# Kernel tuning notes

Hardware: AMD Instinct MI355X
Metric: run time of the kernel (lower is better)

Reference implementation:

```python
import jax, jax.numpy as jnp
import numpy as np
from jax import lax

D_MODEL = 1024
D_STATE = 16
D_CONV = 4
EXPAND = 2
D_INNER = EXPAND * D_MODEL  # 2048
DT_RANK = -(-D_MODEL // 16)  # ceil = 64
BATCH = 2
T = 1024


def setup_inputs() -> dict:
    key = jax.random.key(0)
    ks = jax.random.split(key, 9)
    s = 0.02
    x = jax.random.normal(ks[0], (BATCH, T, D_MODEL), dtype=jnp.float32)
    W_in = jax.random.normal(ks[1], (D_MODEL, 2 * D_INNER), dtype=jnp.float32) * s
    conv_w = jax.random.normal(ks[2], (D_INNER, D_CONV), dtype=jnp.float32) * 0.2
    conv_b = jax.random.normal(ks[3], (D_INNER,), dtype=jnp.float32) * 0.02
    W_xproj = jax.random.normal(ks[4], (D_INNER, DT_RANK + 2 * D_STATE), dtype=jnp.float32) * s
    W_dt = jax.random.normal(ks[5], (DT_RANK, D_INNER), dtype=jnp.float32) * s
    b_dt = jax.random.normal(ks[6], (D_INNER,), dtype=jnp.float32) * 0.02
    A_log = jnp.broadcast_to(jnp.log(jnp.arange(1, D_STATE + 1, dtype=jnp.float32)), (D_INNER, D_STATE)).copy()
    D_param = jnp.ones((D_INNER,), dtype=jnp.float32)
    W_out = jax.random.normal(ks[7], (D_INNER, D_MODEL), dtype=jnp.float32) * s
    return {"x": x, "W_in": W_in, "conv_w": conv_w, "conv_b": conv_b,
            "W_xproj": W_xproj, "W_dt": W_dt, "b_dt": b_dt,
            "A_log": A_log, "D_param": D_param, "W_out": W_out}


def _silu(u):
    return u * jax.nn.sigmoid(u)


def _forward(x, W_in, conv_w, conv_b, W_xproj, W_dt, b_dt, A_log, D_param, W_out):
    B, Tlen, _ = x.shape
    # in_proj and split into x-branch and gate z
    xz = x @ W_in                                   # (B,T,2*d_inner)
    x_b, z = jnp.split(xz, 2, axis=-1)              # each (B,T,d_inner)
    # causal depthwise conv1d: y[t] = sum_k w[:,k] * x[t-d_conv+1+k]
    xpad = jnp.pad(x_b, ((0, 0), (D_CONV - 1, 0), (0, 0)))
    xc = conv_b
    for k in range(D_CONV):
        xc = xc + xpad[:, k:k + Tlen, :] * conv_w[:, k]
    xc = _silu(xc)                                  # (B,T,d_inner)
    # SSM parameter projections
    proj = xc @ W_xproj                             # (B,T,dt_rank+2*d_state)
    delta_raw = proj[..., :DT_RANK]
    B_in = proj[..., DT_RANK:DT_RANK + D_STATE]     # (B,T,d_state)
    C_in = proj[..., DT_RANK + D_STATE:]            # (B,T,d_state)
    delta = jax.nn.softplus(delta_raw @ W_dt + b_dt)  # (B,T,d_inner)
    A = -jnp.exp(A_log)                             # (d_inner,d_state)
    A_bar = jnp.exp(delta[..., None] * A)           # (B,T,d_inner,d_state)
    Bx = delta[..., None] * B_in[:, :, None, :] * xc[..., None]  # (B,T,d_inner,d_state)

    def step(h, ins):
        a_t, bx_t, c_t, xc_t = ins
        h = a_t * h + bx_t                          # (B,d_inner,d_state)
        y_t = jnp.einsum('bds,bs->bd', h, c_t) + D_param * xc_t
        return h, y_t

    h0 = jnp.zeros((B, D_INNER, D_STATE), dtype=x.dtype)
    ins = (jnp.swapaxes(A_bar, 0, 1), jnp.swapaxes(Bx, 0, 1),
           jnp.swapaxes(C_in, 0, 1), jnp.swapaxes(xc, 0, 1))
    _, ys = lax.scan(step, h0, ins)                 # ys: (T,B,d_inner)
    y = jnp.swapaxes(ys, 0, 1) * _silu(z)           # gated
    return y @ W_out                                # (B,T,d_model)


def reference(x, W_in, conv_w, conv_b, W_xproj, W_dt, b_dt, A_log, D_param, W_out):
    return _forward(x, W_in, conv_w, conv_b, W_xproj, W_dt, b_dt, A_log, D_param, W_out)
```

## Files before the change

### kernel.cpp

```cpp
#include <hip/hip_runtime.h>
#include <math.h>

#define BATCH   2
#define TLEN    1024
#define DMODEL  1024
#define DINNER  2048
#define DSTATE  16
#define DTRANK  64
#define NPROJ   (DTRANK + 2*DSTATE)
#define CH      16
#define NCH     (TLEN / CH)

typedef __attribute__((ext_vector_type(8))) short short8;
typedef __attribute__((ext_vector_type(4))) float f32x4;

__device__ __forceinline__ float siluf(float u) {
    return u / (1.0f + __expf(-u));
}
__device__ __forceinline__ float softplusf(float x) {
    return (x > 20.0f) ? x : log1pf(__expf(x));
}
__device__ __forceinline__ unsigned short f2bf(float f) {
    union { float f; unsigned u; } v; v.f = f;
    unsigned r = v.u + 0x7FFF + ((v.u >> 16) & 1);
    return (unsigned short)(r >> 16);
}

#define GLOAD_LDS16(g, l) \
  __builtin_amdgcn_global_load_lds( \
     (const __attribute__((address_space(1))) unsigned int*)(g), \
     (__attribute__((address_space(3))) unsigned int*)(l), 16, 0, 0)

template<int NFRAG>
__global__ __launch_bounds__(256)
void gemm_bf16(const unsigned short* __restrict__ A,
               const unsigned short* __restrict__ BT,
               float* __restrict__ C, int ldc, int K)
{
    constexpr int BN = NFRAG * 32;
    __shared__ unsigned short As[128 * 32];
    __shared__ unsigned short Bs[BN * 32];

    const int tid  = threadIdx.x;
    const int wid  = tid >> 6;
    const int lane = tid & 63;
    const int brow = blockIdx.y * 128;
    const int bcol = blockIdx.x * BN;
    const int wr = (wid >> 1) * 64;
    const int wc = (wid & 1) * (NFRAG * 16);
    const int lrow = lane & 15;
    const int lk   = (lane >> 4) * 8;

    f32x4 acc[4][NFRAG] = {};

    for (int k0 = 0; k0 < K; k0 += 32) {
        #pragma unroll
        for (int it = 0; it < 2; ++it) {
            const int c = it * 256 + tid;
            const unsigned short* g = A + (size_t)(brow + (c >> 2)) * K + k0 + (c & 3) * 8;
            GLOAD_LDS16(g, As + (size_t)(it * 256 + wid * 64) * 8);
        }
        #pragma unroll
        for (int it = 0; it < BN / 64; ++it) {
            const int c = it * 256 + tid;
            const unsigned short* g = BT + (size_t)(bcol + (c >> 2)) * K + k0 + (c & 3) * 8;
            GLOAD_LDS16(g, Bs + (size_t)(it * 256 + wid * 64) * 8);
        }
        __syncthreads();

        short8 af[4], bfr[NFRAG];
        #pragma unroll
        for (int m = 0; m < 4; ++m)
            af[m] = *(const short8*)(As + (size_t)(wr + m * 16 + lrow) * 32 + lk);
        #pragma unroll
        for (int n = 0; n < NFRAG; ++n)
            bfr[n] = *(const short8*)(Bs + (size_t)(wc + n * 16 + lrow) * 32 + lk);

        #pragma unroll
        for (int m = 0; m < 4; ++m)
            #pragma unroll
            for (int n = 0; n < NFRAG; ++n)
                acc[m][n] = __builtin_amdgcn_mfma_f32_16x16x32_bf16(af[m], bfr[n], acc[m][n], 0, 0, 0);
        __syncthreads();
    }

    const int crow = (lane >> 4) * 4;
    #pragma unroll
    for (int m = 0; m < 4; ++m)
        #pragma unroll
        for (int n = 0; n < NFRAG; ++n) {
            float* cp = C + (size_t)(brow + wr + m * 16 + crow) * ldc + bcol + wc + n * 16 + lrow;
            #pragma unroll
            for (int r = 0; r < 4; ++r)
                cp[(size_t)r * ldc] = acc[m][n][r];
        }
}

template<int EPI>
__global__ __launch_bounds__(256)
void gemm_f32(const float* __restrict__ A, int lda,
              const float* __restrict__ B, int ldb,
              float* __restrict__ C, int ldc,
              int N, int kchunk,
              const float* __restrict__ bias, size_t zstride)
{
    __shared__ float As[16][64 + 4];
    __shared__ float Bs[16][64 + 4];
    const int tid  = threadIdx.x;
    const int brow = blockIdx.y * 64;
    const int bcol = blockIdx.x * 64;
    const int kbeg = blockIdx.z * kchunk;
    C += (size_t)blockIdx.z * zstride;
    const int tr = ((tid >> 4) & 15) << 2;
    const int tc = (tid & 15) << 2;
    const int ar = tid >> 2;
    const int ac = (tid & 3) << 2;
    const int br = tid >> 4;
    const int bc = (tid & 15) << 2;

    float acc[4][4] = {{0.f,0.f,0.f,0.f},{0.f,0.f,0.f,0.f},
                       {0.f,0.f,0.f,0.f},{0.f,0.f,0.f,0.f}};

    for (int k0 = kbeg; k0 < kbeg + kchunk; k0 += 16) {
        float4 av = *(const float4*)(A + (size_t)(brow + ar) * lda + k0 + ac);
        As[ac+0][ar] = av.x; As[ac+1][ar] = av.y;
        As[ac+2][ar] = av.z; As[ac+3][ar] = av.w;

        float4 bv = make_float4(0.f, 0.f, 0.f, 0.f);
        if (bcol + bc < N)
            bv = *(const float4*)(B + (size_t)(k0 + br) * ldb + bcol + bc);
        *(float4*)&Bs[br][bc] = bv;

        __syncthreads();
        #pragma unroll
        for (int k = 0; k < 16; ++k) {
            float4 a4 = *(const float4*)&As[k][tr];
            float4 b4 = *(const float4*)&Bs[k][tc];
            float am[4] = {a4.x, a4.y, a4.z, a4.w};
            float bn[4] = {b4.x, b4.y, b4.z, b4.w};
            #pragma unroll
            for (int m = 0; m < 4; ++m)
                #pragma unroll
                for (int n = 0; n < 4; ++n)
                    acc[m][n] = fmaf(am[m], bn[n], acc[m][n]);
        }
        __syncthreads();
    }

    #pragma unroll
    for (int m = 0; m < 4; ++m) {
        const int gr = brow + tr + m;
        #pragma unroll
        for (int n = 0; n < 4; ++n) {
            const int gc = bcol + tc + n;
            if (gc < N) {
                float v = acc[m][n];
                if (EPI == 1) v = softplusf(v + bias[gc]);
                C[(size_t)gr * ldc + gc] = v;
            }
        }
    }
}

__global__ __launch_bounds__(256)
void reduce8(const float* __restrict__ in, float* __restrict__ out, int n, size_t zstride)
{
    const int i = blockIdx.x * 256 + threadIdx.x;
    if (i >= n) return;
    float s = 0.f;
    #pragma unroll
    for (int z = 0; z < 8; ++z) s += in[(size_t)z * zstride + i];
    out[i] = s;
}

__global__ __launch_bounds__(256)
void cast_rn(const float* __restrict__ in, unsigned short* __restrict__ out)
{
    const int i = blockIdx.x * 256 + threadIdx.x;
    float4 v = ((const float4*)in)[i];
    union { unsigned short u[4]; uint2 v2; } o;
    o.u[0] = f2bf(v.x); o.u[1] = f2bf(v.y); o.u[2] = f2bf(v.z); o.u[3] = f2bf(v.w);
    ((uint2*)out)[i] = o.v2;
}

__global__ __launch_bounds__(256)
void transpose_cast(const float* __restrict__ in, unsigned short* __restrict__ out,
                    int R, int C)
{
    __shared__ float tile[32][33];
    const int tx = threadIdx.x & 31, ty = threadIdx.x >> 5;
    const int c0 = blockIdx.x * 32, r0 = blockIdx.y * 32;
    #pragma unroll
    for (int j = 0; j < 32; j += 8)
        tile[ty + j][tx] = in[(size_t)(r0 + ty + j) * C + c0 + tx];
    __syncthreads();
    #pragma unroll
    for (int j = 0; j < 32; j += 8)
        out[(size_t)(c0 + ty + j) * R + r0 + tx] = f2bf(tile[tx][ty + j]);
}

__global__ __launch_bounds__(256)
void conv_silu(const float* __restrict__ xz, const float* __restrict__ conv_w,
               const float* __restrict__ conv_b, float* __restrict__ xc)
{
    const int idx = blockIdx.x * 256 + threadIdx.x;
    const int d = idx & (DINNER - 1);
    const int t = (idx >> 11) & (TLEN - 1);
    const int b = idx >> 21;

    const float* xb = xz + (size_t)b * TLEN * (2*DINNER) + d;
    float s = conv_b[d];
    const float4 w = *(const float4*)(conv_w + d * 4);
    const float wk[4] = {w.x, w.y, w.z, w.w};
    #pragma unroll
    for (int k = 0; k < 4; ++k) {
        const int tt = t + k - 3;
        if (tt >= 0) s = fmaf(xb[(size_t)tt * (2*DINNER)], wk[k], s);
    }
    xc[idx] = siluf(s);
}

__global__ __launch_bounds__(256)
void scan1(const float* __restrict__ delta, const float* __restrict__ xc,
           const float* __restrict__ proj, const float* __restrict__ A_log,
           float* __restrict__ hloc, float* __restrict__ sumdel)
{
    const int idx = blockIdx.x * 256 + threadIdx.x;
    const int d = idx & (DINNER - 1);
    const int c = (idx >> 11) & (NCH - 1);
    const int b = idx >> 17;

    float Aa[DSTATE];
    #pragma unroll
    for (int s = 0; s < DSTATE; ++s) Aa[s] = -__expf(A_log[d * DSTATE + s]);

    float h[DSTATE];
    #pragma unroll
    for (int s = 0; s < DSTATE; ++s) h[s] = 0.f;
    float sd = 0.f;

    const int t0 = c * CH;
    const float* dptr = delta + ((size_t)(b * TLEN + t0)) * DINNER + d;
    const float* xptr = xc    + ((size_t)(b * TLEN + t0)) * DINNER + d;
    const float* pptr = proj  + ((size_t)(b * TLEN + t0)) * NPROJ;

    for (int t = 0; t < CH; ++t) {
        const float dl = dptr[(size_t)t * DINNER];
        const float xv = xptr[(size_t)t * DINNER];
        const float dx = dl * xv;
        sd += dl;
        #pragma unroll
        for (int s = 0; s < DSTATE; ++s) {
            const float ab = __expf(dl * Aa[s]);
            const float Bv = pptr[t * NPROJ + DTRANK + s];
            h[s] = fmaf(ab, h[s], dx * Bv);
        }
    }
    const size_t base = (((size_t)(b * DINNER + d)) * NCH + c) * DSTATE;
    float4* hp = (float4*)(hloc + base);
    hp[0] = make_float4(h[0],  h[1],  h[2],  h[3]);
    hp[1] = make_float4(h[4],  h[5],  h[6],  h[7]);
    hp[2] = make_float4(h[8],  h[9],  h[10], h[11]);
    hp[3] = make_float4(h[12], h[13], h[14], h[15]);
    sumdel[(size_t)(b * DINNER + d) * NCH + c] = sd;
}

__global__ __launch_bounds__(256)
void scan_combine(const float* __restrict__ hloc, const float* __restrict__ sumdel,
                  const float* __restrict__ A_log, float* __restrict__ hstart)
{
    __shared__ float hl[64 * 17];
    __shared__ float hs[64 * 17];
    const int bd   = blockIdx.x;
    const int d    = bd & (DINNER - 1);
    const int tid  = threadIdx.x;
    const int lane = tid & 63;
    const int w    = tid >> 6;

    const size_t gbase = (size_t)bd * NCH * DSTATE;
    {
        const float4 v = ((const float4*)(hloc + gbase))[tid];
        const int c = tid >> 2, s0 = (tid & 3) * 4;
        hl[c*17 + s0+0] = v.x; hl[c*17 + s0+1] = v.y;
        hl[c*17 + s0+2] = v.z; hl[c*17 + s0+3] = v.w;
    }
    const float sd = sumdel[(size_t)bd * NCH + lane];
    __syncthreads();

    #pragma unroll
    for (int q = 0; q < 4; ++q) {
        const int s = w * 4 + q;
        const float Aa = -__expf(A_log[d * DSTATE + s]);
        float A  = __expf(Aa * sd);
        float Bv = hl[lane*17 + s];
        #pragma unroll
        for (int off = 1; off < 64; off <<= 1) {
            float Ap = __shfl_up(A, off);
            float Bp = __shfl_up(Bv, off);
            if (lane >= off) { Bv = fmaf(A, Bp, Bv); A *= Ap; }
        }
        float hsv = __shfl_up(Bv, 1);
        if (lane == 0) hsv = 0.f;
        hs[lane*17 + s] = hsv;
    }
    __syncthreads();
    {
        const int c = tid >> 2, s0 = (tid & 3) * 4;
        float4 v = make_float4(hs[c*17 + s0+0], hs[c*17 + s0+1],
                               hs[c*17 + s0+2], hs[c*17 + s0+3]);
        ((float4*)(hstart + gbase))[tid] = v;
    }
}

__global__ __launch_bounds__(256)
void scan2(const float* __restrict__ delta, const float* __restrict__ xc,
           const float* __restrict__ proj, const float* __restrict__ A_log,
           const float* __restrict__ D_param, const float* __restrict__ xz,
           const float* __restrict__ hstart, unsigned short* __restrict__ y)
{
    const int idx = blockIdx.x * 256 + threadIdx.x;
    const int d = idx & (DINNER - 1);
    const int c = (idx >> 11) & (NCH - 1);
    const int b = idx >> 17;

    float Aa[DSTATE];
    #pragma unroll
    for (int s = 0; s < DSTATE; ++s) Aa[s] = -__expf(A_log[d * DSTATE + s]);

    float h[DSTATE];
    const size_t hbase = (((size_t)(b * DINNER + d)) * NCH + c) * DSTATE;
    {
        const float4* hp = (const float4*)(hstart + hbase);
        float4 v0 = hp[0], v1 = hp[1], v2 = hp[2], v3 = hp[3];
        h[0]=v0.x; h[1]=v0.y; h[2]=v0.z; h[3]=v0.w;
        h[4]=v1.x; h[5]=v1.y; h[6]=v1.z; h[7]=v1.w;
        h[8]=v2.x; h[9]=v2.y; h[10]=v2.z; h[11]=v2.w;
        h[12]=v3.x; h[13]=v3.y; h[14]=v3.z; h[15]=v3.w;
    }

    const float Dp = D_param[d];
    const int t0 = c * CH;
    const float* dptr = delta + ((size_t)(b * TLEN + t0)) * DINNER + d;
    const float* xptr = xc    + ((size_t)(b * TLEN + t0)) * DINNER + d;
    const float* pptr = proj  + ((size_t)(b * TLEN + t0)) * NPROJ;
    const float* zptr = xz + ((size_t)(b * TLEN + t0)) * (2*DINNER) + DINNER + d;
    unsigned short* yptr = y + ((size_t)(b * TLEN + t0)) * DINNER + d;

    for (int t = 0; t < CH; ++t) {
        const float dl = dptr[(size_t)t * DINNER];
        const float xv = xptr[(size_t)t * DINNER];
        const float dx = dl * xv;
        float yt = 0.f;
        #pragma unroll
        for (int s = 0; s < DSTATE; ++s) {
            const float ab = __expf(dl * Aa[s]);
            const float Bv = pptr[t * NPROJ + DTRANK + s];
            h[s] = fmaf(ab, h[s], dx * Bv);
            const float Cv = pptr[t * NPROJ + DTRANK + DSTATE + s];
            yt = fmaf(h[s], Cv, yt);
        }
        yt = fmaf(Dp, xv, yt);
        const float z = zptr[(size_t)t * (2*DINNER)];
        yptr[(size_t)t * DINNER] = f2bf(yt * siluf(z));
    }
}

extern "C" void kernel_launch(void* const* d_in, const int* in_sizes, int n_in,
                              void* d_out, int out_size, void* d_ws, size_t ws_size,
                              hipStream_t stream)
{
    const float* x      = (const float*)d_in[0];
    const float* W_in   = (const float*)d_in[1];
    const float* conv_w = (const float*)d_in[2];
    const float* conv_b = (const float*)d_in[3];
    const float* W_xproj= (const float*)d_in[4];
    const float* W_dt   = (const float*)d_in[5];
    const float* b_dt   = (const float*)d_in[6];
    const float* A_log  = (const float*)d_in[7];
    const float* D_param= (const float*)d_in[8];
    const float* W_out  = (const float*)d_in[9];
    float* out = (float*)d_out;

    float* ws = (float*)d_ws;
    float* xz     = ws;
    float* xc     = xz     + 8388608;
    float* proj   = xc     + 4194304;
    float* delta  = proj   + 196608;
    float* hloc   = delta  + 4194304;
    float* sumdel = hloc   + 4194304;
    float* hstart = sumdel + 262144;
    float* projp  = hloc;
    unsigned short* x_bf  = (unsigned short*)hstart;
    unsigned short* wt_in = (unsigned short*)(hstart + 1048576);
    unsigned short* yb_bf = (unsigned short*)hloc;
    unsigned short* wt_out= (unsigned short*)(hloc + 2097152);

    dim3 blk(256);

    cast_rn<<<(BATCH*TLEN*DMODEL/4)/256, blk, 0, stream>>>(x, x_bf);
    transpose_cast<<<dim3(2*DINNER/32, DMODEL/32), blk, 0, stream>>>(W_in, wt_in, DMODEL, 2*DINNER);
    gemm_bf16<4><<<dim3(2*DINNER/128, 2048/128), blk, 0, stream>>>(x_bf, wt_in, xz, 2*DINNER, DMODEL);

    conv_silu<<<(BATCH*TLEN*DINNER)/256, blk, 0, stream>>>(xz, conv_w, conv_b, xc);

    gemm_f32<0><<<dim3(2, 2048/64, 8), blk, 0, stream>>>(
        xc, DINNER, W_xproj, NPROJ, projp, NPROJ, NPROJ, DINNER/8, nullptr, 196608);
    reduce8<<<(196608 + 255)/256, blk, 0, stream>>>(projp, proj, 196608, 196608);

    gemm_f32<1><<<dim3(2048/64, 2048/64), blk, 0, stream>>>(
        proj, NPROJ, W_dt, DINNER, delta, DINNER, DINNER, DTRANK, b_dt, 0);

    scan1<<<(BATCH*NCH*DINNER)/256, blk, 0, stream>>>(delta, xc, proj, A_log, hloc, sumdel);
    scan_combine<<<BATCH*DINNER, blk, 0, stream>>>(hloc, sumdel, A_log, hstart);
    transpose_cast<<<dim3(DMODEL/32, DINNER/32), blk, 0, stream>>>(W_out, wt_out, DINNER, DMODEL);
    scan2<<<(BATCH*NCH*DINNER)/256, blk, 0, stream>>>(delta, xc, proj, A_log, D_param, xz, hstart, yb_bf);

    gemm_bf16<2><<<dim3(DMODEL/64, 2048/128), blk, 0, stream>>>(yb_bf, wt_out, out, DMODEL, DINNER);
}
```

Measured before the change: 289.7 us.

## Store xz, xc and delta intermediates in bf16 and remap GEMM blocks per XCD

The large intermediates (in_proj output xz, conv output xc, delta) are now stored as bf16 instead of fp32. This halves the memory traffic of the conv, scan and projection kernels, which are bandwidth-bound. The bf16 GEMM also remaps workgroup IDs so consecutive tiles land on the same XCD for better L2 locality. The cost is lower precision in the scan inputs, which could affect accuracy tolerance.

```diff
diff --git a/kernel.cpp b/kernel.cpp
--- a/kernel.cpp
+++ b/kernel.cpp
@@ -25,27 +25,39 @@
     unsigned r = v.u + 0x7FFF + ((v.u >> 16) & 1);
     return (unsigned short)(r >> 16);
 }
+__device__ __forceinline__ float bf2f(unsigned short u) {
+    union { unsigned u; float f; } v; v.u = (unsigned)u << 16;
+    return v.f;
+}
 
 #define GLOAD_LDS16(g, l) \
   __builtin_amdgcn_global_load_lds( \
      (const __attribute__((address_space(1))) unsigned int*)(g), \
      (__attribute__((address_space(3))) unsigned int*)(l), 16, 0, 0)
 
-template<int NFRAG>
+template<int NFRAG, int OUTBF>
 __global__ __launch_bounds__(256)
 void gemm_bf16(const unsigned short* __restrict__ A,
                const unsigned short* __restrict__ BT,
-               float* __restrict__ C, int ldc, int K)
+               void* __restrict__ Cv, int ldc, int K)
 {
     constexpr int BN = NFRAG * 32;
     __shared__ unsigned short As[128 * 32];
     __shared__ unsigned short Bs[BN * 32];
 
+    const int nwg = gridDim.x * gridDim.y;
+    int id = blockIdx.y * gridDim.x + blockIdx.x;
+    {
+        const int q = nwg >> 3, r = nwg & 7, xcd = id & 7, lid = id >> 3;
+        id = (xcd < r ? xcd * (q + 1) : r * (q + 1) + (xcd - r) * q) + lid;
+    }
+    const int bx = id % gridDim.x, by = id / gridDim.x;
+
     const int tid  = threadIdx.x;
     const int wid  = tid >> 6;
     const int lane = tid & 63;
-    const int brow = blockIdx.y * 128;
-    const int bcol = blockIdx.x * BN;
+    const int brow = by * 128;
+    const int bcol = bx * BN;
     const int wr = (wid >> 1) * 64;
     const int wc = (wid & 1) * (NFRAG * 16);
     const int lrow = lane & 15;
@@ -89,18 +101,22 @@
     for (int m = 0; m < 4; ++m)
         #pragma unroll
         for (int n = 0; n < NFRAG; ++n) {
-            float* cp = C + (size_t)(brow + wr + m * 16 + crow) * ldc + bcol + wc + n * 16 + lrow;
+            const size_t coff = (size_t)(brow + wr + m * 16 + crow) * ldc + bcol + wc + n * 16 + lrow;
             #pragma unroll
-            for (int r = 0; r < 4; ++r)
-                cp[(size_t)r * ldc] = acc[m][n][r];
-        }
-}
-
-template<int EPI>
-__global__ __launch_bounds__(256)
-void gemm_f32(const float* __restrict__ A, int lda,
+            for (int r = 0; r < 4; ++r) {
+                if (OUTBF)
+                    ((unsigned short*)Cv)[coff + (size_t)r * ldc] = f2bf(acc[m][n][r]);
+                else
+                    ((float*)Cv)[coff + (size_t)r * ldc] = acc[m][n][r];
+            }
+        }
+}
+
+template<int EPI, int ABF, int OUTBF>
+__global__ __launch_bounds__(256)
+void gemm_f32(const void* __restrict__ Av, int lda,
               const float* __restrict__ B, int ldb,
-              float* __restrict__ C, int ldc,
+              void* __restrict__ Cv, int ldc,
               int N, int kchunk,
               const float* __restrict__ bias, size_t zstride)
 {
@@ -110,7 +126,7 @@
     const int brow = blockIdx.y * 64;
     const int bcol = blockIdx.x * 64;
     const int kbeg = blockIdx.z * kchunk;
-    C += (size_t)blockIdx.z * zstride;
+    const size_t cofs = (size_t)blockIdx.z * zstride;
     const int tr = ((tid >> 4) & 15) << 2;
     const int tc = (tid & 15) << 2;
     const int ar = tid >> 2;
@@ -122,7 +138,14 @@
                        {0.f,0.f,0.f,0.f},{0.f,0.f,0.f,0.f}};
 
     for (int k0 = kbeg; k0 < kbeg + kchunk; k0 += 16) {
-        float4 av = *(const float4*)(A + (size_t)(brow + ar) * lda + k0 + ac);
+        float4 av;
+        if (ABF) {
+            const unsigned short* Ab = (const unsigned short*)Av;
+            ushort4 t = *(const ushort4*)(Ab + (size_t)(brow + ar) * lda + k0 + ac);
+            av = make_float4(bf2f(t.x), bf2f(t.y), bf2f(t.z), bf2f(t.w));
+        } else {
+            av = *(const float4*)((const float*)Av + (size_t)(brow + ar) * lda + k0 + ac);
+        }
         As[ac+0][ar] = av.x; As[ac+1][ar] = av.y;
         As[ac+2][ar] = av.z; As[ac+3][ar] = av.w;
 
@@ -156,7 +179,10 @@
             if (gc < N) {
                 float v = acc[m][n];
                 if (EPI == 1) v = softplusf(v + bias[gc]);
-                C[(size_t)gr * ldc + gc] = v;
+                if (OUTBF)
+                    ((unsigned short*)Cv)[cofs + (size_t)gr * ldc + gc] = f2bf(v);
+                else
+                    ((float*)Cv)[cofs + (size_t)gr * ldc + gc] = v;
             }
         }
     }
@@ -200,28 +226,28 @@
 }
 
 __global__ __launch_bounds__(256)
-void conv_silu(const float* __restrict__ xz, const float* __restrict__ conv_w,
-               const float* __restrict__ conv_b, float* __restrict__ xc)
+void conv_silu(const unsigned short* __restrict__ xz, const float* __restrict__ conv_w,
+               const float* __restrict__ conv_b, unsigned short* __restrict__ xc)
 {
     const int idx = blockIdx.x * 256 + threadIdx.x;
     const int d = idx & (DINNER - 1);
     const int t = (idx >> 11) & (TLEN - 1);
     const int b = idx >> 21;
 
-    const float* xb = xz + (size_t)b * TLEN * (2*DINNER) + d;
+    const unsigned short* xb = xz + (size_t)b * TLEN * (2*DINNER) + d;
     float s = conv_b[d];
     const float4 w = *(const float4*)(conv_w + d * 4);
     const float wk[4] = {w.x, w.y, w.z, w.w};
     #pragma unroll
     for (int k = 0; k < 4; ++k) {
         const int tt = t + k - 3;
-        if (tt >= 0) s = fmaf(xb[(size_t)tt * (2*DINNER)], wk[k], s);
-    }
-    xc[idx] = siluf(s);
-}
-
-__global__ __launch_bounds__(256)
-void scan1(const float* __restrict__ delta, const float* __restrict__ xc,
+        if (tt >= 0) s = fmaf(bf2f(xb[(size_t)tt * (2*DINNER)]), wk[k], s);
+    }
+    xc[idx] = f2bf(siluf(s));
+}
+
+__global__ __launch_bounds__(256)
+void scan1(const unsigned short* __restrict__ delta, const unsigned short* __restrict__ xc,
            const float* __restrict__ proj, const float* __restrict__ A_log,
            float* __restrict__ hloc, float* __restrict__ sumdel)
 {
@@ -240,13 +266,13 @@
     float sd = 0.f;
 
     const int t0 = c * CH;
-    const float* dptr = delta + ((size_t)(b * TLEN + t0)) * DINNER + d;
-    const float* xptr = xc    + ((size_t)(b * TLEN + t0)) * DINNER + d;
+    const unsigned short* dptr = delta + ((size_t)(b * TLEN + t0)) * DINNER + d;
+    const unsigned short* xptr = xc    + ((size_t)(b * TLEN + t0)) * DINNER + d;
     const float* pptr = proj  + ((size_t)(b * TLEN + t0)) * NPROJ;
 
     for (int t = 0; t < CH; ++t) {
-        const float dl = dptr[(size_t)t * DINNER];
-        const float xv = xptr[(size_t)t * DINNER];
+        const float dl = bf2f(dptr[(size_t)t * DINNER]);
+        const float xv = bf2f(xptr[(size_t)t * DINNER]);
         const float dx = dl * xv;
         sd += dl;
         #pragma unroll
@@ -313,9 +339,9 @@
 }
 
 __global__ __launch_bounds__(256)
-void scan2(const float* __restrict__ delta, const float* __restrict__ xc,
+void scan2(const unsigned short* __restrict__ delta, const unsigned short* __restrict__ xc,
            const float* __restrict__ proj, const float* __restrict__ A_log,
-           const float* __restrict__ D_param, const float* __restrict__ xz,
+           const float* __restrict__ D_param, const unsigned short* __restrict__ xz,
            const float* __restrict__ hstart, unsigned short* __restrict__ y)
 {
     const int idx = blockIdx.x * 256 + threadIdx.x;
@@ -340,15 +366,15 @@
 
     const float Dp = D_param[d];
     const int t0 = c * CH;
-    const float* dptr = delta + ((size_t)(b * TLEN + t0)) * DINNER + d;
-    const float* xptr = xc    + ((size_t)(b * TLEN + t0)) * DINNER + d;
+    const unsigned short* dptr = delta + ((size_t)(b * TLEN + t0)) * DINNER + d;
+    const unsigned short* xptr = xc    + ((size_t)(b * TLEN + t0)) * DINNER + d;
     const float* pptr = proj  + ((size_t)(b * TLEN + t0)) * NPROJ;
-    const float* zptr = xz + ((size_t)(b * TLEN + t0)) * (2*DINNER) + DINNER + d;
+    const unsigned short* zptr = xz + ((size_t)(b * TLEN + t0)) * (2*DINNER) + DINNER + d;
     unsigned short* yptr = y + ((size_t)(b * TLEN + t0)) * DINNER + d;
 
     for (int t = 0; t < CH; ++t) {
-        const float dl = dptr[(size_t)t * DINNER];
-        const float xv = xptr[(size_t)t * DINNER];
+        const float dl = bf2f(dptr[(size_t)t * DINNER]);
+        const float xv = bf2f(xptr[(size_t)t * DINNER]);
         const float dx = dl * xv;
         float yt = 0.f;
         #pragma unroll
@@ -360,7 +386,7 @@
             yt = fmaf(h[s], Cv, yt);
         }
         yt = fmaf(Dp, xv, yt);
-        const float z = zptr[(size_t)t * (2*DINNER)];
+        const float z = bf2f(zptr[(size_t)t * (2*DINNER)]);
         yptr[(size_t)t * DINNER] = f2bf(yt * siluf(z));
     }
 }
@@ -382,38 +408,38 @@
     float* out = (float*)d_out;
 
     float* ws = (float*)d_ws;
-    float* xz     = ws;
-    float* xc     = xz     + 8388608;
-    float* proj   = xc     + 4194304;
-    float* delta  = proj   + 196608;
-    float* hloc   = delta  + 4194304;
-    float* sumdel = hloc   + 4194304;
-    float* hstart = sumdel + 262144;
-    float* projp  = hloc;
-    unsigned short* x_bf  = (unsigned short*)hstart;
-    unsigned short* wt_in = (unsigned short*)(hstart + 1048576);
-    unsigned short* yb_bf = (unsigned short*)hloc;
-    unsigned short* wt_out= (unsigned short*)(hloc + 2097152);
+    unsigned short* xz_bf    = (unsigned short*)ws;
+    unsigned short* xc_bf    = (unsigned short*)(ws + 4194304);
+    float*          proj     = ws + 6291456;
+    unsigned short* delta_bf = (unsigned short*)(ws + 6488064);
+    float*          hloc     = ws + 8585216;
+    float*          sumdel   = ws + 12779520;
+    float*          hstart   = ws + 13041664;
+    float*          projp    = hloc;
+    unsigned short* x_bf     = (unsigned short*)hstart;
+    unsigned short* wt_in    = (unsigned short*)(hstart + 1048576);
+    unsigned short* yb_bf    = (unsigned short*)hloc;
+    unsigned short* wt_out   = (unsigned short*)(hloc + 2097152);
 
     dim3 blk(256);
 
     cast_rn<<<(BATCH*TLEN*DMODEL/4)/256, blk, 0, stream>>>(x, x_bf);
     transpose_cast<<<dim3(2*DINNER/32, DMODEL/32), blk, 0, stream>>>(W_in, wt_in, DMODEL, 2*DINNER);
-    gemm_bf16<4><<<dim3(2*DINNER/128, 2048/128), blk, 0, stream>>>(x_bf, wt_in, xz, 2*DINNER, DMODEL);
-
-    conv_silu<<<(BATCH*TLEN*DINNER)/256, blk, 0, stream>>>(xz, conv_w, conv_b, xc);
-
-    gemm_f32<0><<<dim3(2, 2048/64, 8), blk, 0, stream>>>(
-        xc, DINNER, W_xproj, NPROJ, projp, NPROJ, NPROJ, DINNER/8, nullptr, 196608);
+    gemm_bf16<4,1><<<dim3(2*DINNER/128, 2048/128), blk, 0, stream>>>(x_bf, wt_in, xz_bf, 2*DINNER, DMODEL);
+
+    conv_silu<<<(BATCH*TLEN*DINNER)/256, blk, 0, stream>>>(xz_bf, conv_w, conv_b, xc_bf);
+
+    gemm_f32<0,1,0><<<dim3(2, 2048/64, 8), blk, 0, stream>>>(
+        xc_bf, DINNER, W_xproj, NPROJ, projp, NPROJ, NPROJ, DINNER/8, nullptr, 196608);
     reduce8<<<(196608 + 255)/256, blk, 0, stream>>>(projp, proj, 196608, 196608);
 
-    gemm_f32<1><<<dim3(2048/64, 2048/64), blk, 0, stream>>>(
-        proj, NPROJ, W_dt, DINNER, delta, DINNER, DINNER, DTRANK, b_dt, 0);
-
-    scan1<<<(BATCH*NCH*DINNER)/256, blk, 0, stream>>>(delta, xc, proj, A_log, hloc, sumdel);
+    gemm_f32<1,0,1><<<dim3(2048/64, 2048/64), blk, 0, stream>>>(
+        proj, NPROJ, W_dt, DINNER, delta_bf, DINNER, DINNER, DTRANK, b_dt, 0);
+
+    scan1<<<(BATCH*NCH*DINNER)/256, blk, 0, stream>>>(delta_bf, xc_bf, proj, A_log, hloc, sumdel);
     scan_combine<<<BATCH*DINNER, blk, 0, stream>>>(hloc, sumdel, A_log, hstart);
     transpose_cast<<<dim3(DMODEL/32, DINNER/32), blk, 0, stream>>>(W_out, wt_out, DINNER, DMODEL);
-    scan2<<<(BATCH*NCH*DINNER)/256, blk, 0, stream>>>(delta, xc, proj, A_log, D_param, xz, hstart, yb_bf);
-
-    gemm_bf16<2><<<dim3(DMODEL/64, 2048/128), blk, 0, stream>>>(yb_bf, wt_out, out, DMODEL, DINNER);
-}
+    scan2<<<(BATCH*NCH*DINNER)/256, blk, 0, stream>>>(delta_bf, xc_bf, proj, A_log, D_param, xz_bf, hstart, yb_bf);
+
+    gemm_bf16<2,0><<<dim3(DMODEL/64, 2048/128), blk, 0, stream>>>(yb_bf, wt_out, out, DMODEL, DINNER);
+}
```

New measurement: 291.1 us. About the same (+0.5%).
